# Optimization experiments

Measured on AMD Instinct MI355X. Metric: run time of the kernel, lower is better.

Reference implementation:

```python
import jax, jax.numpy as jnp
import numpy as np
import math

B, S, DM, H, F = 2, 2048, 1024, 16, 192  # F = head_dim init arg; per-head dim = F // 3
DH = F // 3
MAX_BIAS = 8.0


def _get_slopes(n):
    # faithful to ALiBiBias._get_slopes
    def pow2(n):
        start = 2.0 ** (-(2.0 ** (-(math.log2(n) - 3))))
        return [start * start ** i for i in range(n)]
    if math.log2(n).is_integer():
        return pow2(n)
    cp2 = 2 ** math.floor(math.log2(n))
    return pow2(cp2) + _get_slopes(2 * cp2)[0::2][: n - cp2]


def _rope_sin_cos(seq_len, dim):
    inv_freq = 1.0 / (10000.0 ** (jnp.arange(0, dim, 2, dtype=jnp.float32) / dim))
    freqs = jnp.outer(jnp.arange(seq_len, dtype=jnp.float32), inv_freq)  # [S, dim/2]
    # repeat(sin[:,None,:],2,axis=1).reshape(S,-1) == concat([sin,sin],-1)
    sin = jnp.concatenate([jnp.sin(freqs), jnp.sin(freqs)], axis=-1)  # [S, dim]
    cos = jnp.concatenate([jnp.cos(freqs), jnp.cos(freqs)], axis=-1)
    return sin, cos


def _rotate_half(x):
    x1, x2 = jnp.split(x, 2, axis=-1)
    return jnp.concatenate([-x2, x1], axis=-1)


def setup_inputs() -> dict:
    key = jax.random.key(0)
    kx, kq, ko = jax.random.split(key, 3)
    x = jax.random.normal(kx, (B, S, DM), dtype=jnp.float32)
    w_qkv = jax.random.normal(kq, (DM, H, F), dtype=jnp.float32) * (1.0 / math.sqrt(DM))
    b_qkv = jnp.zeros((H, F), dtype=jnp.float32)
    w_out = jax.random.normal(ko, (H, DH, DM), dtype=jnp.float32) * (1.0 / math.sqrt(H * DH))
    b_out = jnp.zeros((DM,), dtype=jnp.float32)
    return {"x": x, "w_qkv": w_qkv, "b_qkv": b_qkv, "w_out": w_out, "b_out": b_out}


def reference(x, w_qkv, b_qkv, w_out, b_out):
    b, s, dm = x.shape
    h, f = w_qkv.shape[1], w_qkv.shape[2]
    dh = f // 3
    # fused QKV projection: [B,S,H,F], then 3-way split on the feature axis
    qkv = jnp.einsum('bsd,dhf->bshf', x, w_qkv) + b_qkv
    q, k, v = jnp.split(qkv, 3, axis=-1)  # each [B,S,H,DH]
    # RoPE (rotate_half convention), broadcast over heads
    sin, cos = _rope_sin_cos(s, dh)
    sin, cos = sin[:, None, :], cos[:, None, :]  # [S,1,DH]
    q = q * cos + _rotate_half(q) * sin
    k = k * cos + _rotate_half(k) * sin
    # [B,H,S,DH]
    q = q.transpose(0, 2, 1, 3)
    k = k.transpose(0, 2, 1, 3)
    v = v.transpose(0, 2, 1, 3)
    # scores scaled by sqrt(head_dim init arg), as in the original non-flash path
    scores = jnp.einsum('bhqd,bhkd->bhqk', q, k) / jnp.sqrt(jnp.float32(f))
    # ALiBi bias
    slopes = jnp.asarray(_get_slopes(h), dtype=jnp.float32)  # [H]
    pos = jnp.arange(s, dtype=jnp.float32)
    rel = pos[None, :] - pos[:, None]  # j - i
    rel = jnp.where(rel > 0, 0.0, rel)
    alibi = rel[None, :, :] * slopes[:, None, None] * MAX_BIAS  # [H,S,S]
    scores = scores + alibi[None]  # [B,H,S,S]
    # causal mask
    causal = jnp.tril(jnp.ones((s, s), dtype=jnp.float32))
    scores = jnp.where(causal == 0, -1e9, scores)
    weights = jax.nn.softmax(scores, axis=-1)
    attn = jnp.einsum('bhqk,bhkd->bhqd', weights, v).transpose(0, 2, 1, 3)  # [B,S,H,DH]
    return jnp.einsum('bshd,hdm->bsm', attn, w_out) + b_out
```

## Files before the change

kernel.cpp:

```cpp
#include <hip/hip_runtime.h>
#include <math.h>

static constexpr int B_  = 2;
static constexpr int S_  = 2048;
static constexpr int H_  = 16;
static constexpr int DH_ = 64;
static constexpr float QSCALE2_ = 0.104117589f;
static constexpr float C8L2_    = 11.5415603f;

typedef __attribute__((ext_vector_type(8))) short short8;
typedef __attribute__((ext_vector_type(4))) float floatx4;

__device__ __forceinline__ float bf2f(unsigned short u) {
    union { unsigned int i; float f; } c; c.i = ((unsigned int)u) << 16; return c.f;
}
__device__ __forceinline__ unsigned short f2bf(float f) {
    union { float f; unsigned int i; } c; c.f = f;
    unsigned int x = c.i;
    unsigned int r = (x + 0x7fffu + ((x >> 16) & 1u)) >> 16;
    if ((x & 0x7f800000u) == 0x7f800000u) r = x >> 16;
    return (unsigned short)r;
}
__device__ __forceinline__ void load_lds16(const unsigned short* g, unsigned short* l) {
    __builtin_amdgcn_global_load_lds(
        (const __attribute__((address_space(1))) unsigned int*)g,
        (__attribute__((address_space(3))) unsigned int*)l, 16, 0, 0);
}

__global__ __launch_bounds__(256) void prep(
    const float* __restrict__ x,     unsigned short* __restrict__ xb,
    const float* __restrict__ w_qkv, unsigned short* __restrict__ wqkvT,
    const float* __restrict__ w_out, unsigned short* __restrict__ woutT)
{
    __shared__ float t[32][33];
    const int bid = blockIdx.x;
    if (bid < 4096) {
        const int i = bid * 256 + threadIdx.x;
        const float4 v = reinterpret_cast<const float4*>(x)[i];
        ushort4 r;
        r.x = f2bf(v.x); r.y = f2bf(v.y); r.z = f2bf(v.z); r.w = f2bf(v.w);
        reinterpret_cast<ushort4*>(xb)[i] = r;
        return;
    }
    const float* in; unsigned short* out; int NN, bx, by;
    if (bid < 7168) {
        in = w_qkv; out = wqkvT; NN = 3072;
        const int b2 = bid - 4096; bx = b2 % 96; by = b2 / 96;
    } else {
        in = w_out; out = woutT; NN = 1024;
        const int b2 = bid - 7168; bx = b2 & 31; by = b2 >> 5;
    }
    const int n0 = bx * 32;
    const int k0 = by * 32;
    const int tn = threadIdx.x & 31, tk = threadIdx.x >> 5;
    #pragma unroll
    for (int i = 0; i < 4; ++i)
        t[tk + 8 * i][tn] = in[(size_t)(k0 + tk + 8 * i) * NN + n0 + tn];
    __syncthreads();
    #pragma unroll
    for (int i = 0; i < 4; ++i)
        out[(size_t)(n0 + tk + 8 * i) * 1024 + k0 + tn] = f2bf(t[tn][tk + 8 * i]);
}

__global__ __launch_bounds__(256) void gemm_qkv(
    const unsigned short* __restrict__ A, const unsigned short* __restrict__ BT,
    const float* __restrict__ bias,
    unsigned short* __restrict__ O0, unsigned short* __restrict__ O1,
    unsigned short* __restrict__ O2)
{
    __shared__ unsigned short As[128 * 32];
    __shared__ unsigned short Bs[128 * 32];

    const int tid  = threadIdx.x;
    const int wave = tid >> 6;
    const int lane = tid & 63;
    const int quad = lane >> 4;
    const int lm   = lane & 15;
    const int wm = (wave >> 1) * 64;
    const int wn = (wave & 1) * 64;
    const int n0 = blockIdx.x * 128;
    const int m0 = blockIdx.y * 128;

    floatx4 acc[4][4] = {};

    const int sr = lane >> 2;
    const int sc = lane & 3;

    for (int k0 = 0; k0 < 1024; k0 += 32) {
        #pragma unroll
        for (int rep = 0; rep < 2; ++rep) {
            const int r = wave * 32 + rep * 16;
            load_lds16(A  + (size_t)(m0 + r + sr) * 1024 + k0 + sc * 8, &As[r * 32]);
            load_lds16(BT + (size_t)(n0 + r + sr) * 1024 + k0 + sc * 8, &Bs[r * 32]);
        }
        __syncthreads();
        short8 af[4], bf[4];
        #pragma unroll
        for (int i = 0; i < 4; ++i) {
            af[i] = *reinterpret_cast<const short8*>(&As[(wm + i * 16 + lm) * 32 + quad * 8]);
            bf[i] = *reinterpret_cast<const short8*>(&Bs[(wn + i * 16 + lm) * 32 + quad * 8]);
        }
        #pragma unroll
        for (int mi = 0; mi < 4; ++mi)
            #pragma unroll
            for (int ni = 0; ni < 4; ++ni)
                acc[mi][ni] = __builtin_amdgcn_mfma_f32_16x16x32_bf16(
                    af[mi], bf[ni], acc[mi][ni], 0, 0, 0);
        __syncthreads();
    }

    const int nbase = n0 + wn;
    const int h   = nbase / 192;
    const int sec = (nbase - h * 192) >> 6;
    float bia[4];
    #pragma unroll
    for (int ni = 0; ni < 4; ++ni) bia[ni] = bias[nbase + ni * 16 + lm];
    unsigned short* Out = (sec == 0) ? O0 : ((sec == 1) ? O1 : O2);

    if (sec == 2) {
        #pragma unroll
        for (int mi = 0; mi < 4; ++mi) {
            const int m  = m0 + wm + mi * 16 + quad * 4;
            const int bb = m >> 11;
            const int s  = m & (S_ - 1);
            const size_t rowb = (size_t)(bb * H_ + h) * DH_;
            #pragma unroll
            for (int ni = 0; ni < 4; ++ni) {
                const int d = ni * 16 + lm;
                ushort4 w;
                w.x = f2bf(acc[mi][ni][0] + bia[ni]);
                w.y = f2bf(acc[mi][ni][1] + bia[ni]);
                w.z = f2bf(acc[mi][ni][2] + bia[ni]);
                w.w = f2bf(acc[mi][ni][3] + bia[ni]);
                *reinterpret_cast<ushort4*>(&Out[(rowb + d) * S_ + s]) = w;
            }
        }
    } else {
        const float qscale = (sec == 0) ? QSCALE2_ : 1.0f;
        const float nlf = -13.287712379549449f / 32.0f;
        const float invf0 = exp2f((float)lm * nlf);
        const float invf1 = exp2f((float)(lm + 16) * nlf);
        #pragma unroll
        for (int mi = 0; mi < 4; ++mi) {
            #pragma unroll
            for (int r = 0; r < 4; ++r) {
                const int m  = m0 + wm + mi * 16 + quad * 4 + r;
                const int bb = m >> 11;
                const int s  = m & (S_ - 1);
                const size_t obase = ((size_t)(bb * H_ + h) * S_ + s) * DH_;
                const float a0 = (float)s * invf0, a1 = (float)s * invf1;
                const float sn0 = __sinf(a0), cs0 = __cosf(a0);
                const float sn1 = __sinf(a1), cs1 = __cosf(a1);
                #pragma unroll
                for (int ni = 0; ni < 4; ++ni) {
                    const int d = ni * 16 + lm;
                    const float v = acc[mi][ni][r]     + bia[ni];
                    const float p = acc[mi][ni ^ 2][r] + bia[ni ^ 2];
                    const float cs = (ni & 1) ? cs1 : cs0;
                    const float sn = (ni & 1) ? sn1 : sn0;
                    float res = (d < 32) ? (v * cs - p * sn) : (v * cs + p * sn);
                    Out[obase + d] = f2bf(res * qscale);
                }
            }
        }
    }
}

__global__ __launch_bounds__(256) void gemm_out(
    const unsigned short* __restrict__ A, const unsigned short* __restrict__ BT,
    const float* __restrict__ bias, float* __restrict__ Of)
{
    __shared__ unsigned short As[64 * 32];
    __shared__ unsigned short Bs[128 * 32];

    const int tid  = threadIdx.x;
    const int wave = tid >> 6;
    const int lane = tid & 63;
    const int quad = lane >> 4;
    const int lm   = lane & 15;
    const int wm = (wave >> 1) * 32;
    const int wn = (wave & 1) * 64;
    const int n0 = blockIdx.x * 128;
    const int m0 = blockIdx.y * 64;

    floatx4 acc[2][4] = {};

    const int sr = lane >> 2;
    const int sc = lane & 3;

    for (int k0 = 0; k0 < 1024; k0 += 32) {
        load_lds16(A + (size_t)(m0 + wave * 16 + sr) * 1024 + k0 + sc * 8,
                   &As[wave * 16 * 32]);
        #pragma unroll
        for (int rep = 0; rep < 2; ++rep) {
            const int r = wave * 32 + rep * 16;
            load_lds16(BT + (size_t)(n0 + r + sr) * 1024 + k0 + sc * 8, &Bs[r * 32]);
        }
        __syncthreads();
        short8 af[2], bf[4];
        #pragma unroll
        for (int i = 0; i < 2; ++i)
            af[i] = *reinterpret_cast<const short8*>(&As[(wm + i * 16 + lm) * 32 + quad * 8]);
        #pragma unroll
        for (int i = 0; i < 4; ++i)
            bf[i] = *reinterpret_cast<const short8*>(&Bs[(wn + i * 16 + lm) * 32 + quad * 8]);
        #pragma unroll
        for (int mi = 0; mi < 2; ++mi)
            #pragma unroll
            for (int ni = 0; ni < 4; ++ni)
                acc[mi][ni] = __builtin_amdgcn_mfma_f32_16x16x32_bf16(
                    af[mi], bf[ni], acc[mi][ni], 0, 0, 0);
        __syncthreads();
    }

    #pragma unroll
    for (int ni = 0; ni < 4; ++ni) {
        const int gn = n0 + wn + ni * 16 + lm;
        const float b = bias[gn];
        #pragma unroll
        for (int mi = 0; mi < 2; ++mi) {
            const int gm = m0 + wm + mi * 16 + quad * 4;
            #pragma unroll
            for (int r = 0; r < 4; ++r)
                Of[(size_t)(gm + r) * 1024 + gn] = acc[mi][ni][r] + b;
        }
    }
}

static constexpr int KST = 68;
static constexpr int PST = 68;

__global__ __launch_bounds__(512, 4) void flash_mfma(
    const unsigned short* __restrict__ Q, const unsigned short* __restrict__ K,
    const unsigned short* __restrict__ VT, unsigned short* __restrict__ Ao)
{
    __shared__ unsigned short Ks[2][64 * KST];
    __shared__ unsigned short VTs[2][64 * KST];
    __shared__ unsigned short Ps[8][16 * PST];

    const int bi = blockIdx.x;
    const int bh = bi & 31;
    const int p  = bi >> 5;
    const int h  = bh & 15;
    const int b  = bh >> 4;
    const int tid  = threadIdx.x;
    const int wave = tid >> 6;
    const int lane = tid & 63;
    const int quad = lane >> 4;
    const int lm   = lane & 15;
    const int wq   = wave & 3;
    const int qt   = (wave < 4) ? (31 - p) : p;
    const int nkt  = 32 - p;
    const int srow = tid >> 3;
    const int sc8  = tid & 7;

    const unsigned short* Kg  = K  + (size_t)bh * S_ * DH_;
    const unsigned short* VTg = VT + (size_t)bh * DH_ * S_;

    const float slope2 = exp2f(-0.5f * (float)(h + 1)) * (8.0f * 1.44269504f);
    const float d64 = 64.0f * slope2;

    int   koff[4];
    float alb[4];
    #pragma unroll
    for (int t = 0; t < 4; ++t) {
        koff[t] = t * 16 + quad * 4 - wq * 16 - lm;
        alb[t]  = (float)koff[t] * slope2 - C8L2_;
    }

    unsigned short* Pw = &Ps[wave][0];

    const unsigned short* Qrow =
        Q + ((size_t)bh * S_ + (size_t)(qt * 64 + wq * 16 + lm)) * DH_;
    const short8 aq0 = *reinterpret_cast<const short8*>(Qrow + quad * 8);
    const short8 aq1 = *reinterpret_cast<const short8*>(Qrow + 32 + quad * 8);

    float crk[4];
    #pragma unroll
    for (int r = 0; r < 4; ++r)
        crk[r] = (float)r * slope2 - (float)qt * d64;

    float l_one = 0.0f;
    floatx4 acc_o[4] = {};

    short8 ka, va;
    ka = *reinterpret_cast<const short8*>(Kg + (size_t)srow * DH_ + sc8 * 8);
    va = *reinterpret_cast<const short8*>(VTg + (size_t)srow * S_ + sc8 * 8);
    *reinterpret_cast<short8*>(&Ks[0][srow * KST + sc8 * 8])  = ka;
    *reinterpret_cast<short8*>(&VTs[0][srow * KST + sc8 * 8]) = va;
    ka = *reinterpret_cast<const short8*>(Kg + (size_t)(64 + srow) * DH_ + sc8 * 8);
    va = *reinterpret_cast<const short8*>(VTg + (size_t)srow * S_ + 64 + sc8 * 8);
    __syncthreads();

    for (int kt = 0; kt < nkt; ++kt) {
        const int cur = kt & 1;

        if (kt + 1 < nkt) {
            const int nxt = cur ^ 1;
            *reinterpret_cast<short8*>(&Ks[nxt][srow * KST + sc8 * 8])  = ka;
            *reinterpret_cast<short8*>(&VTs[nxt][srow * KST + sc8 * 8]) = va;
            if (kt + 2 < nkt) {
                ka = *reinterpret_cast<const short8*>(
                    Kg + (size_t)((kt + 2) * 64 + srow) * DH_ + sc8 * 8);
                va = *reinterpret_cast<const short8*>(
                    VTg + (size_t)srow * S_ + (kt + 2) * 64 + sc8 * 8);
            }
        }

        if (kt <= qt) {
            floatx4 sacc[4] = {};
            __builtin_amdgcn_s_setprio(1);
            #pragma unroll
            for (int t = 0; t < 4; ++t) {
                const short8 k0 = *reinterpret_cast<const short8*>(&Ks[cur][(t * 16 + lm) * KST + quad * 8]);
                const short8 k1 = *reinterpret_cast<const short8*>(&Ks[cur][(t * 16 + lm) * KST + 32 + quad * 8]);
                sacc[t] = __builtin_amdgcn_mfma_f32_16x16x32_bf16(k0, aq0, sacc[t], 0, 0, 0);
                sacc[t] = __builtin_amdgcn_mfma_f32_16x16x32_bf16(k1, aq1, sacc[t], 0, 0, 0);
            }
            __builtin_amdgcn_s_setprio(0);

            const bool diag = (kt == qt);
            #pragma unroll
            for (int t = 0; t < 4; ++t) {
                float pv[4];
                #pragma unroll
                for (int r = 0; r < 4; ++r) {
                    const float x = (sacc[t][r] + alb[t]) + crk[r];
                    float e;
                    asm("v_exp_f32 %0, %1" : "=v"(e) : "v"(x));
                    if (diag && (koff[t] + r) > 0) e = 0.0f;
                    pv[r] = e;
                }
                l_one += (pv[0] + pv[1]) + (pv[2] + pv[3]);
                unsigned int lo, hi;
                asm("v_cvt_pk_bf16_f32 %0, %1, %2" : "=v"(lo) : "v"(pv[0]), "v"(pv[1]));
                asm("v_cvt_pk_bf16_f32 %0, %1, %2" : "=v"(hi) : "v"(pv[2]), "v"(pv[3]));
                uint2 w; w.x = lo; w.y = hi;
                *reinterpret_cast<uint2*>(&Pw[lm * PST + t * 16 + quad * 4]) = w;
            }
            #pragma unroll
            for (int r = 0; r < 4; ++r) crk[r] += d64;

            const short8 ap0 = *reinterpret_cast<const short8*>(&Pw[lm * PST + quad * 8]);
            const short8 ap1 = *reinterpret_cast<const short8*>(&Pw[lm * PST + 32 + quad * 8]);
            __builtin_amdgcn_s_setprio(1);
            #pragma unroll
            for (int t = 0; t < 4; ++t) {
                const short8 v0 = *reinterpret_cast<const short8*>(&VTs[cur][(t * 16 + lm) * KST + quad * 8]);
                const short8 v1 = *reinterpret_cast<const short8*>(&VTs[cur][(t * 16 + lm) * KST + 32 + quad * 8]);
                acc_o[t] = __builtin_amdgcn_mfma_f32_16x16x32_bf16(ap0, v0, acc_o[t], 0, 0, 0);
                acc_o[t] = __builtin_amdgcn_mfma_f32_16x16x32_bf16(ap1, v1, acc_o[t], 0, 0, 0);
            }
            __builtin_amdgcn_s_setprio(0);
        }
        __syncthreads();
    }

    l_one += __shfl_xor(l_one, 16);
    l_one += __shfl_xor(l_one, 32);
    #pragma unroll
    for (int r = 0; r < 4; ++r) {
        const float lr = __shfl(l_one, quad * 4 + r);
        const float inv_l = 1.0f / lr;
        const int s = qt * 64 + wq * 16 + quad * 4 + r;
        const size_t obase = ((size_t)(b * S_ + s) * H_ + h) * DH_;
        #pragma unroll
        for (int t = 0; t < 4; ++t)
            Ao[obase + t * 16 + lm] = f2bf(acc_o[t][r] * inv_l);
    }
}

extern "C" void kernel_launch(void* const* d_in, const int* in_sizes, int n_in,
                              void* d_out, int out_size, void* d_ws, size_t ws_size,
                              hipStream_t stream)
{
    const float *x = nullptr, *w_qkv = nullptr, *b_qkv = nullptr,
                *w_out = nullptr, *b_out = nullptr;
    for (int i = 0; i < n_in; ++i) {
        switch (in_sizes[i]) {
            case 4194304: x     = (const float*)d_in[i]; break;
            case 3145728: w_qkv = (const float*)d_in[i]; break;
            case 3072:    b_qkv = (const float*)d_in[i]; break;
            case 1048576: w_out = (const float*)d_in[i]; break;
            case 1024:    b_out = (const float*)d_in[i]; break;
        }
    }
    if (!x)     x     = (const float*)d_in[0];
    if (!w_qkv) w_qkv = (const float*)d_in[1];
    if (!b_qkv) b_qkv = (const float*)d_in[2];
    if (!w_out) w_out = (const float*)d_in[3];
    if (!b_out) b_out = (const float*)d_in[4];

    float* out = (float*)d_out;
    unsigned short* ws16 = (unsigned short*)d_ws;

    unsigned short* xb     = ws16;
    unsigned short* wqkvT  = ws16 + (size_t)4194304;
    unsigned short* woutT  = ws16 + (size_t)7340032;
    unsigned short* Qb     = ws16 + (size_t)8388608;
    unsigned short* Kb     = ws16 + (size_t)12582912;
    unsigned short* Vb     = ws16 + (size_t)16777216;
    unsigned short* Aob    = ws16 + (size_t)20971520;

    prep<<<8192, 256, 0, stream>>>(x, xb, w_qkv, wqkvT, w_out, woutT);

    gemm_qkv<<<dim3(24, 32), 256, 0, stream>>>(
        xb, wqkvT, b_qkv, Qb, Kb, Vb);
    flash_mfma<<<dim3(512), 512, 0, stream>>>(Qb, Kb, Vb, Aob);
    gemm_out<<<dim3(8, 64), 256, 0, stream>>>(Aob, woutT, b_out, out);
}
```

Baseline: 186.9 us.

## Split key tiles across two wave groups per query tile with LDS merge

Each block previously processed two mirrored query tiles to balance causal work. Now each block owns a single query tile, and its two 4-wave groups take alternating even and odd key tiles. The partial outputs and row sums are combined through LDS at the end. The grid doubles to 1024 blocks and the launch-bounds occupancy hint rises from 4 to 6. This aims to shorten each block's serial key loop and raise parallelism, at the cost of per-block load imbalance across query tiles, a second barrier per iteration and a final reduction.

Measured after the change: 208.7 us. +11.7%, slower.

```diff
diff --git a/kernel.cpp b/kernel.cpp
--- a/kernel.cpp
+++ b/kernel.cpp
@@ -230,27 +230,27 @@
 static constexpr int KST = 68;
 static constexpr int PST = 68;
 
-__global__ __launch_bounds__(512, 4) void flash_mfma(
+__global__ __launch_bounds__(512, 6) void flash_mfma(
     const unsigned short* __restrict__ Q, const unsigned short* __restrict__ K,
     const unsigned short* __restrict__ VT, unsigned short* __restrict__ Ao)
 {
     __shared__ unsigned short Ks[2][64 * KST];
-    __shared__ unsigned short VTs[2][64 * KST];
+    __shared__ unsigned short Vs[2][64 * KST];
     __shared__ unsigned short Ps[8][16 * PST];
 
-    const int bi = blockIdx.x;
-    const int bh = bi & 31;
-    const int p  = bi >> 5;
-    const int h  = bh & 15;
-    const int b  = bh >> 4;
+    const int bid = blockIdx.x;
+    const int qt  = 31 - (bid >> 5);
+    const int bh  = bid & 31;
+    const int h   = bh & 15;
+    const int b   = bh >> 4;
     const int tid  = threadIdx.x;
     const int wave = tid >> 6;
     const int lane = tid & 63;
     const int quad = lane >> 4;
     const int lm   = lane & 15;
+    const int grp  = wave >> 2;
     const int wq   = wave & 3;
-    const int qt   = (wave < 4) ? (31 - p) : p;
-    const int nkt  = 32 - p;
+    const int niter = (qt + 2) >> 1;
     const int srow = tid >> 3;
     const int sc8  = tid & 7;
 
@@ -258,7 +258,8 @@
     const unsigned short* VTg = VT + (size_t)bh * DH_ * S_;
 
     const float slope2 = exp2f(-0.5f * (float)(h + 1)) * (8.0f * 1.44269504f);
-    const float d64 = 64.0f * slope2;
+    const float d64  = 64.0f * slope2;
+    const float d128 = 2.0f * d64;
 
     int   koff[4];
     float alb[4];
@@ -278,48 +279,44 @@
     float crk[4];
     #pragma unroll
     for (int r = 0; r < 4; ++r)
-        crk[r] = (float)r * slope2 - (float)qt * d64;
+        crk[r] = (float)r * slope2 - (float)qt * d64 + (float)grp * d64;
 
     float l_one = 0.0f;
     floatx4 acc_o[4] = {};
 
-    short8 ka, va;
-    ka = *reinterpret_cast<const short8*>(Kg + (size_t)srow * DH_ + sc8 * 8);
-    va = *reinterpret_cast<const short8*>(VTg + (size_t)srow * S_ + sc8 * 8);
-    *reinterpret_cast<short8*>(&Ks[0][srow * KST + sc8 * 8])  = ka;
-    *reinterpret_cast<short8*>(&VTs[0][srow * KST + sc8 * 8]) = va;
-    ka = *reinterpret_cast<const short8*>(Kg + (size_t)(64 + srow) * DH_ + sc8 * 8);
-    va = *reinterpret_cast<const short8*>(VTg + (size_t)srow * S_ + 64 + sc8 * 8);
+    short8 ke, ko, ve, vo;
+    ke = *reinterpret_cast<const short8*>(Kg + (size_t)srow * DH_ + sc8 * 8);
+    ko = *reinterpret_cast<const short8*>(Kg + (size_t)(64 + srow) * DH_ + sc8 * 8);
+    ve = *reinterpret_cast<const short8*>(VTg + (size_t)srow * S_ + sc8 * 8);
+    vo = *reinterpret_cast<const short8*>(VTg + (size_t)srow * S_ + 64 + sc8 * 8);
+    *reinterpret_cast<short8*>(&Ks[0][srow * KST + sc8 * 8]) = ke;
+    *reinterpret_cast<short8*>(&Ks[1][srow * KST + sc8 * 8]) = ko;
+    *reinterpret_cast<short8*>(&Vs[0][srow * KST + sc8 * 8]) = ve;
+    *reinterpret_cast<short8*>(&Vs[1][srow * KST + sc8 * 8]) = vo;
+    if (niter > 1) {
+        ke = *reinterpret_cast<const short8*>(Kg + (size_t)(128 + srow) * DH_ + sc8 * 8);
+        ko = *reinterpret_cast<const short8*>(Kg + (size_t)(192 + srow) * DH_ + sc8 * 8);
+        ve = *reinterpret_cast<const short8*>(VTg + (size_t)srow * S_ + 128 + sc8 * 8);
+        vo = *reinterpret_cast<const short8*>(VTg + (size_t)srow * S_ + 192 + sc8 * 8);
+    }
     __syncthreads();
 
-    for (int kt = 0; kt < nkt; ++kt) {
-        const int cur = kt & 1;
-
-        if (kt + 1 < nkt) {
-            const int nxt = cur ^ 1;
-            *reinterpret_cast<short8*>(&Ks[nxt][srow * KST + sc8 * 8])  = ka;
-            *reinterpret_cast<short8*>(&VTs[nxt][srow * KST + sc8 * 8]) = va;
-            if (kt + 2 < nkt) {
-                ka = *reinterpret_cast<const short8*>(
-                    Kg + (size_t)((kt + 2) * 64 + srow) * DH_ + sc8 * 8);
-                va = *reinterpret_cast<const short8*>(
-                    VTg + (size_t)srow * S_ + (kt + 2) * 64 + sc8 * 8);
-            }
-        }
-
-        if (kt <= qt) {
+    for (int i = 0; i < niter; ++i) {
+        const int ktg = 2 * i + grp;
+
+        if (ktg <= qt) {
             floatx4 sacc[4] = {};
             __builtin_amdgcn_s_setprio(1);
             #pragma unroll
             for (int t = 0; t < 4; ++t) {
-                const short8 k0 = *reinterpret_cast<const short8*>(&Ks[cur][(t * 16 + lm) * KST + quad * 8]);
-                const short8 k1 = *reinterpret_cast<const short8*>(&Ks[cur][(t * 16 + lm) * KST + 32 + quad * 8]);
+                const short8 k0 = *reinterpret_cast<const short8*>(&Ks[grp][(t * 16 + lm) * KST + quad * 8]);
+                const short8 k1 = *reinterpret_cast<const short8*>(&Ks[grp][(t * 16 + lm) * KST + 32 + quad * 8]);
                 sacc[t] = __builtin_amdgcn_mfma_f32_16x16x32_bf16(k0, aq0, sacc[t], 0, 0, 0);
                 sacc[t] = __builtin_amdgcn_mfma_f32_16x16x32_bf16(k1, aq1, sacc[t], 0, 0, 0);
             }
             __builtin_amdgcn_s_setprio(0);
 
-            const bool diag = (kt == qt);
+            const bool diag = (ktg == qt);
             #pragma unroll
             for (int t = 0; t < 4; ++t) {
                 float pv[4];
@@ -339,34 +336,70 @@
                 *reinterpret_cast<uint2*>(&Pw[lm * PST + t * 16 + quad * 4]) = w;
             }
             #pragma unroll
-            for (int r = 0; r < 4; ++r) crk[r] += d64;
+            for (int r = 0; r < 4; ++r) crk[r] += d128;
 
             const short8 ap0 = *reinterpret_cast<const short8*>(&Pw[lm * PST + quad * 8]);
             const short8 ap1 = *reinterpret_cast<const short8*>(&Pw[lm * PST + 32 + quad * 8]);
             __builtin_amdgcn_s_setprio(1);
             #pragma unroll
             for (int t = 0; t < 4; ++t) {
-                const short8 v0 = *reinterpret_cast<const short8*>(&VTs[cur][(t * 16 + lm) * KST + quad * 8]);
-                const short8 v1 = *reinterpret_cast<const short8*>(&VTs[cur][(t * 16 + lm) * KST + 32 + quad * 8]);
+                const short8 v0 = *reinterpret_cast<const short8*>(&Vs[grp][(t * 16 + lm) * KST + quad * 8]);
+                const short8 v1 = *reinterpret_cast<const short8*>(&Vs[grp][(t * 16 + lm) * KST + 32 + quad * 8]);
                 acc_o[t] = __builtin_amdgcn_mfma_f32_16x16x32_bf16(ap0, v0, acc_o[t], 0, 0, 0);
                 acc_o[t] = __builtin_amdgcn_mfma_f32_16x16x32_bf16(ap1, v1, acc_o[t], 0, 0, 0);
             }
             __builtin_amdgcn_s_setprio(0);
         }
         __syncthreads();
-    }
-
-    l_one += __shfl_xor(l_one, 16);
-    l_one += __shfl_xor(l_one, 32);
-    #pragma unroll
-    for (int r = 0; r < 4; ++r) {
-        const float lr = __shfl(l_one, quad * 4 + r);
-        const float inv_l = 1.0f / lr;
-        const int s = qt * 64 + wq * 16 + quad * 4 + r;
-        const size_t obase = ((size_t)(b * S_ + s) * H_ + h) * DH_;
+
+        if (i + 1 < niter) {
+            *reinterpret_cast<short8*>(&Ks[0][srow * KST + sc8 * 8]) = ke;
+            *reinterpret_cast<short8*>(&Ks[1][srow * KST + sc8 * 8]) = ko;
+            *reinterpret_cast<short8*>(&Vs[0][srow * KST + sc8 * 8]) = ve;
+            *reinterpret_cast<short8*>(&Vs[1][srow * KST + sc8 * 8]) = vo;
+            if (i + 2 < niter) {
+                const int e = (i + 2) * 2;
+                ke = *reinterpret_cast<const short8*>(Kg + (size_t)(e * 64 + srow) * DH_ + sc8 * 8);
+                ko = *reinterpret_cast<const short8*>(Kg + (size_t)((e + 1) * 64 + srow) * DH_ + sc8 * 8);
+                ve = *reinterpret_cast<const short8*>(VTg + (size_t)srow * S_ + e * 64 + sc8 * 8);
+                vo = *reinterpret_cast<const short8*>(VTg + (size_t)srow * S_ + (e + 1) * 64 + sc8 * 8);
+            }
+            __syncthreads();
+        }
+    }
+
+    float* mb = reinterpret_cast<float*>(&Ps[0][0]);
+    if (grp == 1) {
+        const int idx = ((wave - 4) * 64 + lane) * 17;
         #pragma unroll
         for (int t = 0; t < 4; ++t)
-            Ao[obase + t * 16 + lm] = f2bf(acc_o[t][r] * inv_l);
+            #pragma unroll
+            for (int r = 0; r < 4; ++r)
+                mb[idx + t * 4 + r] = acc_o[t][r];
+        mb[idx + 16] = l_one;
+    }
+    __syncthreads();
+    if (grp == 0) {
+        const int idx = (wave * 64 + lane) * 17;
+        #pragma unroll
+        for (int t = 0; t < 4; ++t)
+            #pragma unroll
+            for (int r = 0; r < 4; ++r)
+                acc_o[t][r] += mb[idx + t * 4 + r];
+        l_one += mb[idx + 16];
+
+        l_one += __shfl_xor(l_one, 16);
+        l_one += __shfl_xor(l_one, 32);
+        #pragma unroll
+        for (int r = 0; r < 4; ++r) {
+            const float lr = __shfl(l_one, quad * 4 + r);
+            const float inv_l = 1.0f / lr;
+            const int s = qt * 64 + wq * 16 + quad * 4 + r;
+            const size_t obase = ((size_t)(b * S_ + s) * H_ + h) * DH_;
+            #pragma unroll
+            for (int t = 0; t < 4; ++t)
+                Ao[obase + t * 16 + lm] = f2bf(acc_o[t][r] * inv_l);
+        }
     }
 }
 
@@ -406,6 +439,6 @@
 
     gemm_qkv<<<dim3(24, 32), 256, 0, stream>>>(
         xb, wqkvT, b_qkv, Qb, Kb, Vb);
-    flash_mfma<<<dim3(512), 512, 0, stream>>>(Qb, Kb, Vb, Aob);
+    flash_mfma<<<dim3(1024), 512, 0, stream>>>(Qb, Kb, Vb, Aob);
     gemm_out<<<dim3(8, 64), 256, 0, stream>>>(Aob, woutT, b_out, out);
 }
```
